# Kernel tuning notes

Measured on AMD Instinct MI355X. Metric: run time of the kernel, lower is better.

The kernel has to match this reference:

```python
import jax, jax.numpy as jnp
import numpy as np
from functools import partial

DN = ('NCHW', 'OIHW', 'NCHW')

def _conv(x, w, b, stride, pad):
    y = jax.lax.conv_general_dilated(x, w, (stride, stride), [(pad, pad), (pad, pad)], dimension_numbers=DN)
    return y + b[None, :, None, None]

def _leaky(x, s):
    return jnp.where(x >= 0, x, s * x)

def _lstm_gates(pre, c):
    # PyTorch gate order: i, f, g, o
    i, f, g, o = jnp.split(pre, 4, axis=-1)
    c_new = jax.nn.sigmoid(f) * c + jax.nn.sigmoid(i) * jnp.tanh(g)
    h_new = jax.nn.sigmoid(o) * jnp.tanh(c_new)
    return h_new, c_new

def setup_inputs() -> dict:
    key = jax.random.key(0)
    ks = iter(jax.random.split(key, 32))
    s = 0.05
    d = {}
    d['x'] = jax.random.normal(next(ks), (128, 3, 64, 64), jnp.float32)
    # conv stack params
    d['w1'] = jax.random.normal(next(ks), (64, 3, 7, 7)) * s;   d['b1'] = jnp.zeros((64,))
    d['w2'] = jax.random.normal(next(ks), (128, 64, 7, 7)) * s; d['b2'] = jnp.zeros((128,))
    d['w3'] = jax.random.normal(next(ks), (256, 128, 5, 5)) * s; d['b3'] = jnp.zeros((256,))
    d['w4'] = jax.random.normal(next(ks), (512, 256, 5, 5)) * s; d['b4'] = jnp.zeros((512,))
    d['w5'] = jax.random.normal(next(ks), (512, 512, 5, 5)) * s; d['b5'] = jnp.zeros((512,))
    # 2-layer LSTM (hidden=512), PyTorch layout: W_ih [4H, In], W_hh [4H, H]
    H = 512
    for l in range(2):
        d[f'wih{l}'] = jax.random.normal(next(ks), (4 * H, H)) * s
        d[f'whh{l}'] = jax.random.normal(next(ks), (4 * H, H)) * s
        d[f'bih{l}'] = jnp.zeros((4 * H,))
        d[f'bhh{l}'] = jnp.zeros((4 * H,))
    # FC head
    d['fw1'] = jax.random.normal(next(ks), (512, 512)) * s; d['fb1'] = jnp.zeros((512,))
    d['fw2'] = jax.random.normal(next(ks), (13, 512)) * s;  d['fb2'] = jnp.zeros((13,))
    return d

TIMESTEPS = 20

def reference(x, w1, b1, w2, b2, w3, b3, w4, b4, w5, b5,
              wih0, whh0, bih0, bhh0, wih1, whh1, bih1, bhh1,
              fw1, fb1, fw2, fb2):
    B = x.shape[0]
    h = _conv(x, w1, b1, 2, 3); h = _leaky(h, 0.2)
    h = _conv(h, w2, b2, 2, 0); h = _leaky(h, 0.2)
    h = _conv(h, w3, b3, 1, 0); h = _leaky(h, 0.2)
    h = _conv(h, w4, b4, 1, 0); h = _leaky(h, 0.2)
    h = _conv(h, w5, b5, 1, 0); h = _leaky(h, 0.2)
    feat = h.reshape(B, -1)  # [B, 512]
    H = 512
    # input to layer-0 is constant across timesteps: precompute Wx once
    xW0 = feat @ wih0.T + bih0 + bhh0  # [B, 4H]
    zeros = jnp.zeros((B, H), feat.dtype)

    def step(carry, _):
        h0, c0, h1, c1 = carry
        h0n, c0n = _lstm_gates(xW0 + h0 @ whh0.T, c0)
        pre1 = h0n @ wih1.T + bih1 + bhh1 + h1 @ whh1.T
        h1n, c1n = _lstm_gates(pre1, c1)
        return (h0n, c0n, h1n, c1n), h1n

    _, ys = jax.lax.scan(step, (zeros, zeros, zeros, zeros), None, length=TIMESTEPS)
    y = ys.reshape(TIMESTEPS * B, H)
    y = _leaky(y @ fw1.T + fb1, 0.01)
    y = jax.nn.sigmoid(y @ fw2.T + fb2)
    return y
```

## Files before the change

### kernel.cpp

```cpp
#include <hip/hip_runtime.h>
#include <math.h>

typedef _Float16 half_t;
typedef __attribute__((ext_vector_type(8))) _Float16 f16x8;
typedef __attribute__((ext_vector_type(4))) _Float16 f16x4;
typedef __attribute__((ext_vector_type(4))) float f32x4;

#define LEAKY(v, s) ((v) >= 0.f ? (v) : (s) * (v))

__device__ __forceinline__ float sig_(float x) { return 1.f / (1.f + expf(-x)); }
__device__ __forceinline__ half_t f2h(float f) { return (half_t)f; }

#define GLD(gp, lp)                                              \
  __builtin_amdgcn_global_load_lds(                              \
      (const __attribute__((address_space(1))) void*)(gp),       \
      (__attribute__((address_space(3))) void*)(lp), 16, 0, 0)

#define PHASE_WAIT(N)                                            \
  asm volatile("s_waitcnt vmcnt(" #N ")" ::: "memory");          \
  __builtin_amdgcn_s_barrier();                                  \
  __builtin_amdgcn_sched_barrier(0)

#define QOFF0 2048LL
#define QOFF1 4096LL
#define QOFF2 135168LL
#define QOFF3 266240LL
#define QOFF4 5283840LL
#define QOFF5 5310464LL
#define QOFF6 6359040LL
#define QOFF7 6621184LL
#define QOFF8 7669760LL
#define QOFF9 9766912LL

__global__ void prep_all(
    const float* __restrict__ x, const float* __restrict__ w1,
    const float* __restrict__ wih0, const float* __restrict__ whh0,
    const float* __restrict__ bih0, const float* __restrict__ bhh0,
    const float* __restrict__ wih1, const float* __restrict__ whh1,
    const float* __restrict__ bih1, const float* __restrict__ bhh1,
    const float* __restrict__ fw1,
    float* __restrict__ bg0, float* __restrict__ bg1,
    float* __restrict__ czero, unsigned* __restrict__ hzero,
    half_t* __restrict__ xpad, half_t* __restrict__ w1r,
    half_t* __restrict__ wih0h, half_t* __restrict__ fw1h,
    half_t* __restrict__ wcat0h, half_t* __restrict__ wcat1h) {
  long long i = (long long)blockIdx.x * blockDim.x + threadIdx.x;
  if (i < QOFF0) {
    bg0[i] = bih0[i] + bhh0[i];
  } else if (i < QOFF1) {
    long long j = i - QOFF0;
    bg1[j] = bih1[j] + bhh1[j];
  } else if (i < QOFF2) {
    czero[i - QOFF1] = 0.f;
  } else if (i < QOFF3) {
    hzero[i - QOFF2] = 0u;
  } else if (i < QOFF4) {
    long long j = i - QOFF3;
    int c = j & 7;
    long long t = j >> 3;
    int iw = t % 70; t /= 70;
    int ih = t % 70;
    int n = t / 70;
    float v = 0.f;
    if (c < 3 && ih >= 3 && ih < 67 && iw >= 3 && iw < 67)
      v = x[((n * 3 + c) * 64 + (ih - 3)) * 64 + (iw - 3)];
    xpad[j] = f2h(v);
  } else if (i < QOFF5) {
    int j = (int)(i - QOFF4);
    int kg = j % 416, co = j / 416;
    int ci = kg & 7, tap = kg >> 3;
    float v = 0.f;
    if (tap < 49 && ci < 3) {
      int kh = tap / 7, kw = tap % 7;
      v = w1[((co * 3 + ci) * 7 + kh) * 7 + kw];
    }
    w1r[j] = f2h(v);
  } else if (i < QOFF6) {
    int j = (int)(i - QOFF5);
    wih0h[j] = f2h(wih0[j]);
  } else if (i < QOFF7) {
    int j = (int)(i - QOFF6);
    fw1h[j] = f2h(fw1[j]);
  } else if (i < QOFF8) {
    int j = (int)(i - QOFF7);
    int r = j >> 9, k = j & 511;
    int u = r >> 2, g = r & 3;
    wcat0h[j] = f2h(whh0[(g * 512 + u) * 512 + k]);
  } else if (i < QOFF9) {
    int j = (int)(i - QOFF8);
    int r = j >> 10, k = j & 1023;
    int u = r >> 2, g = r & 3;
    int row = g * 512 + u;
    wcat1h[j] = f2h(k < 512 ? wih1[row * 512 + k] : whh1[row * 512 + (k - 512)]);
  }
}

__global__ __launch_bounds__(256) void prep_wT(
    const float* __restrict__ w2, const float* __restrict__ w3,
    const float* __restrict__ w4, const float* __restrict__ w5,
    half_t* __restrict__ w2r, half_t* __restrict__ w3r,
    half_t* __restrict__ w4r, half_t* __restrict__ w5r) {
  __shared__ float T[12800];
  int bid = blockIdx.x, tid = threadIdx.x;
  const float* W;
  half_t* D;
  int co, Cin, TAP, lg2;
  if (bid < 128) {
    W = w2; D = w2r; co = bid; Cin = 64; TAP = 49; lg2 = 6;
  } else if (bid < 384) {
    W = w3; D = w3r; co = bid - 128; Cin = 128; TAP = 25; lg2 = 7;
  } else if (bid < 896) {
    W = w4; D = w4r; co = bid - 384; Cin = 256; TAP = 25; lg2 = 8;
  } else {
    W = w5; D = w5r; co = bid - 896; Cin = 512; TAP = 25; lg2 = 9;
  }
  int n = Cin * TAP;
  const float* src = W + (size_t)co * n;
  for (int i = tid; i < n; i += 256) T[i] = src[i];
  __syncthreads();
  half_t* dst = D + (size_t)co * n;
  for (int j = tid; j < n; j += 256) {
    int ci = j & (Cin - 1);
    int tap = j >> lg2;
    dst[j] = f2h(T[ci * TAP + tap]);
  }
}

template <int KW, int S, int LOG2CIN, int OUTMODE>
__global__ __launch_bounds__(256) void conv_mfma(
    const half_t* __restrict__ xin, const half_t* __restrict__ wr,
    const float* __restrict__ bias, void* __restrict__ outp,
    int Hin, int Win, int Hout, int Wout, int Cout, int K, int ktiles, float slope,
    long long zstride) {
  constexpr int CIN = 1 << LOG2CIN;
  __shared__ half_t lds[4][4096];
  const int tid = threadIdx.x;
  const int lane = tid & 63, wid = tid >> 6;
  const int sRow = tid >> 2, sCh = tid & 3;
  const int sSwz = sCh ^ ((sRow ^ (sRow >> 2)) & 3);
  const int kt0 = blockIdx.z * ktiles;
  const half_t* gArow = wr + (size_t)(blockIdx.y * 64 + sRow) * K + sSwz * 8;
  int p = blockIdx.x * 64 + sRow;
  int hw = Hout * Wout;
  int n = p / hw;
  int rem = p - n * hw;
  int oh = rem / Wout;
  int ow = rem - oh * Wout;
  const half_t* xb = xin + ((size_t)(n * Hin + oh * S) * Win + ow * S) * CIN;
  const int fr = lane & 15, fc = lane >> 4;
  const int r0 = (wid & 1) * 32, c0 = (wid >> 1) * 32;
  const int sw = (fc ^ ((fr ^ (fr >> 2)) & 3)) * 8;
  const int ia0 = (r0 + fr) * 32 + sw;
  const int ia1 = (r0 + 16 + fr) * 32 + sw;
  const int ib0 = 2048 + (c0 + fr) * 32 + sw;
  const int ib1 = 2048 + (c0 + 16 + fr) * 32 + sw;

  auto stage = [&](int t, int buf) {
    GLD(gArow + (size_t)(kt0 + t) * 32, &lds[buf][wid * 512]);
    int kg = (kt0 + t) * 32 + sSwz * 8;
    int ci = kg & (CIN - 1);
    int tap = kg >> LOG2CIN;
    int kh = tap / KW, kw = tap - kh * KW;
    GLD(xb + (kh * Win + kw) * CIN + ci, &lds[buf][2048 + wid * 512]);
  };

  f32x4 acc00 = {0.f, 0.f, 0.f, 0.f};
  f32x4 acc01 = acc00, acc10 = acc00, acc11 = acc00;

// ... 5 lines not shown
    f16x8 b1 = *(const f16x8*)&L[ib1];
    acc00 = __builtin_amdgcn_mfma_f32_16x16x32_f16(a0, b0, acc00, 0, 0, 0);
    acc01 = __builtin_amdgcn_mfma_f32_16x16x32_f16(a0, b1, acc01, 0, 0, 0);
    acc10 = __builtin_amdgcn_mfma_f32_16x16x32_f16(a1, b0, acc10, 0, 0, 0);
    acc11 = __builtin_amdgcn_mfma_f32_16x16x32_f16(a1, b1, acc11, 0, 0, 0);
  };

  stage(0, 0);
  stage(1, 1);
  stage(2, 2);
  int t = 0;
  for (; t < ktiles - 3; ++t) {
    PHASE_WAIT(4);
    stage(t + 3, (t + 3) & 3);
    compute(t & 3);
  }
  PHASE_WAIT(4);
  compute(t & 3);
  ++t;
  PHASE_WAIT(2);
  compute(t & 3);
  ++t;
  PHASE_WAIT(0);
  compute(t & 3);

#pragma unroll
  for (int am = 0; am < 2; ++am) {
#pragma unroll
    for (int bn = 0; bn < 2; ++bn) {
      f32x4 a = am == 0 ? (bn == 0 ? acc00 : acc01) : (bn == 0 ? acc10 : acc11);
      int co = blockIdx.y * 64 + r0 + am * 16 + fc * 4;
      int px = blockIdx.x * 64 + c0 + bn * 16 + fr;
      size_t o = (size_t)px * Cout + co;
      if (OUTMODE == 2) {
        float* pb = (float*)outp + (size_t)blockIdx.z * zstride;
        *(f32x4*)&pb[o] = a;
      } else {
        f32x4 bb = *(const f32x4*)&bias[co];
        f32x4 v;
#pragma unroll
        for (int j = 0; j < 4; ++j) {
          float tt = a[j] + bb[j];
          v[j] = LEAKY(tt, slope);
        }
        if (OUTMODE == 1) {
          *(f32x4*)&((float*)outp)[o] = v;
        } else {
          f16x4 hv;
#pragma unroll
          for (int j = 0; j < 4; ++j) hv[j] = f2h(v[j]);
          *(f16x4*)&((half_t*)outp)[o] = hv;
        }
      }
    }
  }
}

template <int KW, int S, int LOG2CIN, int OUTMODE>
__global__ __launch_bounds__(256) void conv_mfma128(
    const half_t* __restrict__ xin, const half_t* __restrict__ wr,
    const float* __restrict__ bias, void* __restrict__ outp,
    int Hin, int Win, int Hout, int Wout, int Cout, int K, int ktiles, float slope,
    long long zstride, int Y, int G) {
  constexpr int CIN = 1 << LOG2CIN;
  __shared__ half_t lds[4][8192];
  const int L = blockIdx.x;
  const int bx = L / G;
  const int g = L % G;
  const int by = g % Y;
  const int bz = g / Y;
  const int tid = threadIdx.x;
  const int lane = tid & 63, wid = tid >> 6;
  const int sRow = tid >> 2, sCh = tid & 3;
  const int sSwz = sCh ^ ((sRow ^ (sRow >> 2)) & 3);
  const int kt0 = bz * ktiles;
  const half_t* gA0 = wr + (size_t)(by * 128 + sRow) * K + sSwz * 8;
  const half_t* gA1 = wr + (size_t)(by * 128 + 64 + sRow) * K + sSwz * 8;
  int hw = Hout * Wout;
  int p0 = bx * 128 + sRow;
  int n0 = p0 / hw, r0p = p0 - n0 * hw, oh0 = r0p / Wout, ow0 = r0p - oh0 * Wout;
  const half_t* xb0 = xin + ((size_t)(n0 * Hin + oh0 * S) * Win + ow0 * S) * CIN;
  int p1 = p0 + 64;
  int n1 = p1 / hw, r1p = p1 - n1 * hw, oh1 = r1p / Wout, ow1 = r1p - oh1 * Wout;
  const half_t* xb1 = xin + ((size_t)(n1 * Hin + oh1 * S) * Win + ow1 * S) * CIN;

  const int fr = lane & 15, fc = lane >> 4;
  const int wr_ = wid & 1, wc_ = wid >> 1;
  const int sw = (fc ^ ((fr ^ (fr >> 2)) & 3)) * 8;
  const int iaB = (wr_ * 64 + fr) * 32 + sw;
  const int ibB = 4096 + (wc_ * 64 + fr) * 32 + sw;

  auto stage = [&](int t, int buf) {
    half_t* LB = &lds[buf][0];
    GLD(gA0 + (size_t)(kt0 + t) * 32, LB + wid * 512);
    GLD(gA1 + (size_t)(kt0 + t) * 32, LB + 2048 + wid * 512);
    int kg = (kt0 + t) * 32 + sSwz * 8;
    int ci = kg & (CIN - 1);
    int tap = kg >> LOG2CIN;
// ... 18 lines not shown
    for (int fj = 0; fj < 4; ++fj) b[fj] = *(const f16x8*)&L2[ibB + fj * 512];
#pragma unroll
    for (int fi = 0; fi < 4; ++fi)
#pragma unroll
      for (int fj = 0; fj < 4; ++fj)
        acc[fi][fj] = __builtin_amdgcn_mfma_f32_16x16x32_f16(a[fi], b[fj], acc[fi][fj], 0, 0, 0);
  };

  stage(0, 0);
  stage(1, 1);
  stage(2, 2);
  int t = 0;
  for (; t < ktiles - 3; ++t) {
    PHASE_WAIT(8);
    stage(t + 3, (t + 3) & 3);
    compute(t & 3);
  }
  PHASE_WAIT(8);
  compute(t & 3);
  ++t;
  PHASE_WAIT(4);
  compute(t & 3);
  ++t;
  PHASE_WAIT(0);
  compute(t & 3);

#pragma unroll
  for (int fi = 0; fi < 4; ++fi) {
#pragma unroll
    for (int fj = 0; fj < 4; ++fj) {
      int co = by * 128 + wr_ * 64 + fi * 16 + fc * 4;
      int px = bx * 128 + wc_ * 64 + fj * 16 + fr;
      size_t o = (size_t)px * Cout + co;
      if (OUTMODE == 3) {
        half_t* pb = (half_t*)outp + (size_t)bz * zstride;
        f16x4 hv;
#pragma unroll
        for (int j = 0; j < 4; ++j) hv[j] = f2h(acc[fi][fj][j]);
        *(f16x4*)&pb[o] = hv;
      } else {
        f32x4 bb = *(const f32x4*)&bias[co];
        f16x4 hv;
#pragma unroll
        for (int j = 0; j < 4; ++j) {
          float tt = acc[fi][fj][j] + bb[j];
          hv[j] = f2h(LEAKY(tt, slope));
        }
        *(f16x4*)&((half_t*)outp)[o] = hv;
      }
    }
  }
}

__global__ void finalize_part(const float* __restrict__ pb, const float* __restrict__ bias,
                              half_t* __restrict__ out, int size, int nz) {
  int i = blockIdx.x * blockDim.x + threadIdx.x;
  if (i >= size) return;
  float s = bias[i & 511];
  for (int z = 0; z < nz; ++z) s += pb[(size_t)z * size + i];
  out[i] = f2h(LEAKY(s, 0.2f));
}

__global__ void finalize_h(const half_t* __restrict__ pb, const float* __restrict__ bias,
                           half_t* __restrict__ out, int size8, int nz, int cmask,
                           long long zstride) {
  int idx = blockIdx.x * blockDim.x + threadIdx.x;
  if (idx >= size8) return;
  long long i = (long long)idx * 8;
  float s[8];
#pragma unroll
  for (int q = 0; q < 8; ++q) s[q] = bias[(int)((i + q) & cmask)];
  for (int z = 0; z < nz; ++z) {
    f16x8 v = *(const f16x8*)&pb[(size_t)z * zstride + i];
#pragma unroll
    for (int q = 0; q < 8; ++q) s[q] += (float)v[q];
  }
  f16x8 o;
#pragma unroll
  for (int q = 0; q < 8; ++q) o[q] = f2h(LEAKY(s[q], 0.2f));
  *(f16x8*)&out[i] = o;
}

__global__ __launch_bounds__(256) void lstm_fused(
    const half_t* __restrict__ h0in, half_t* __restrict__ h0out,
    const half_t* __restrict__ h1in, half_t* __restrict__ h1out,
    const half_t* __restrict__ wcat0, const half_t* __restrict__ wcat1,
    const float* __restrict__ xw0, const float* __restrict__ bg1,
    float* __restrict__ c0, float* __restrict__ c1,
    half_t* __restrict__ ysout, int zl1, int zfc,
    const half_t* __restrict__ fcw, const float* __restrict__ fcb,
    const half_t* __restrict__ fcin, half_t* __restrict__ fcout) {
  const int bzp = blockIdx.z;
  const bool isFC = (bzp == zfc);
  const bool isL1 = (bzp == zl1);
  if (isFC && blockIdx.y >= 8) return;
  const int NT = isL1 ? 16 : 8;
  const half_t* Asrc = isFC ? fcw : (isL1 ? wcat1 : wcat0);
  const int K = NT * 64;

  __shared__ half_t lds[4][8192];
  const int tid = threadIdx.x;
  const int lane = tid & 63, wid = tid >> 6;
  const int ybase = blockIdx.y * 64, bbase = blockIdx.x * 64;
  const int rA0 = wid * 16 + (lane >> 3);
  const int rA1 = rA0 + 8;
  const int chS = ((lane & 7) ^ ((lane >> 3) & 7)) * 8;
  const half_t* gA0 = Asrc + (size_t)(ybase + rA0) * K + chS;
  const half_t* gA1 = Asrc + (size_t)(ybase + rA1) * K + chS;
  const size_t hb0 = (size_t)(bbase + rA0) * 512 + chS;
  const size_t hb1 = (size_t)(bbase + rA1) * 512 + chS;
  const half_t* bsrc0 = isFC ? fcin : h0in;

  auto stage = [&](int t, int buf) {
    GLD(gA0 + t * 64, &lds[buf][wid * 1024]);
    GLD(gA1 + t * 64, &lds[buf][wid * 1024 + 512]);
    const half_t* hs = (isL1 && t >= 8) ? h1in : bsrc0;
    int koff = (isL1 && t >= 8) ? (t - 8) * 64 : t * 64;
    GLD(hs + hb0 + koff, &lds[buf][4096 + wid * 1024]);
    GLD(hs + hb1 + koff, &lds[buf][4096 + wid * 1024 + 512]);
  };
// ... 47 lines not shown
  ++t;
  PHASE_WAIT(0);
  compute(t & 3);

  if (isFC) {
#pragma unroll
    for (int fi = 0; fi < 2; ++fi) {
#pragma unroll
      for (int fj = 0; fj < 2; ++fj) {
        int Rb = ybase + wr_ * 32 + fi * 16 + fc * 4;
        int b = bbase + wc_ * 32 + fj * 16 + fr;
        f32x4 bb = *(const f32x4*)&fcb[Rb];
        f16x4 hv;
#pragma unroll
        for (int j = 0; j < 4; ++j) {
          float tt = acc[fi][fj][j] + bb[j];
          hv[j] = f2h(LEAKY(tt, 0.01f));
        }
        *(f16x4*)&fcout[(size_t)b * 512 + Rb] = hv;
      }
    }
    return;
  }

  float* c = isL1 ? c1 : c0;
  half_t* hout = isL1 ? h1out : h0out;
#pragma unroll
  for (int fi = 0; fi < 2; ++fi) {
#pragma unroll
    for (int fj = 0; fj < 2; ++fj) {
      int Rb = ybase + wr_ * 32 + fi * 16 + fc * 4;
      int u = Rb >> 2;
      int b = bbase + wc_ * 32 + fj * 16 + fr;
      float p[4];
#pragma unroll
      for (int j = 0; j < 4; ++j) {
        float s = acc[fi][fj][j];
        s += isL1 ? bg1[j * 512 + u] : xw0[b * 2048 + j * 512 + u];
        p[j] = s;
      }
      int ci = b * 512 + u;
      float cprev = c[ci];
      float ig = sig_(p[0]);
      float fg = sig_(p[1]);
      float gg = tanhf(p[2]);
      float og = sig_(p[3]);
      float cn = fg * cprev + ig * gg;
      float hn = og * tanhf(cn);
      c[ci] = cn;
      hout[ci] = f2h(hn);
      if (isL1) ysout[ci] = f2h(hn);
    }
  }
}

__global__ void fc2_sigmoid(const half_t* __restrict__ in, const float* __restrict__ w,
                            const float* __restrict__ b, float* __restrict__ out) {
  int idx = blockIdx.x * blockDim.x + threadIdx.x;
  if (idx >= 2560 * 13) return;
  int j = idx % 13, r = idx / 13;
  const half_t* ip = in + (size_t)r * 512;
  const float* wp = w + j * 512;
  float s = b[j];
  for (int k = 0; k < 512; k += 8) {
    f16x8 hv = *(const f16x8*)&ip[k];
#pragma unroll
    for (int q = 0; q < 8; ++q) s = fmaf((float)hv[q], wp[k + q], s);
  }
  out[idx] = sig_(s);
}

extern "C" void kernel_launch(void* const* d_in, const int* in_sizes, int n_in,
                              void* d_out, int out_size, void* d_ws, size_t ws_size,
                              hipStream_t stream) {
  const float* x   = (const float*)d_in[0];
  const float* w1  = (const float*)d_in[1];  const float* b1 = (const float*)d_in[2];
  const float* w2  = (const float*)d_in[3];  const float* b2 = (const float*)d_in[4];
  const float* w3  = (const float*)d_in[5];  const float* b3 = (const float*)d_in[6];
  const float* w4  = (const float*)d_in[7];  const float* b4 = (const float*)d_in[8];
  const float* w5  = (const float*)d_in[9];  const float* b5 = (const float*)d_in[10];
  const float* wih0 = (const float*)d_in[11]; const float* whh0 = (const float*)d_in[12];
  const float* bih0 = (const float*)d_in[13]; const float* bhh0 = (const float*)d_in[14];
  const float* wih1 = (const float*)d_in[15]; const float* whh1 = (const float*)d_in[16];
  const float* bih1 = (const float*)d_in[17]; const float* bhh1 = (const float*)d_in[18];
  const float* fw1 = (const float*)d_in[19]; const float* fb1 = (const float*)d_in[20];
  const float* fw2 = (const float*)d_in[21]; const float* fb2 = (const float*)d_in[22];
  float* out = (float*)d_out;

  float* bg0 = (float*)d_ws;
  float* bg1 = bg0 + 2048;
  float* xw0 = bg1 + 2048;
  float* c0  = xw0 + 262144;
  float* c1  = c0 + 65536;
  half_t* h0a = (half_t*)(c1 + 65536);
  half_t* h0b = h0a + 65536;
  half_t* h1a = h0b + 65536;
  half_t* h1b = h1a + 65536;
  half_t* BUF1 = h1b + 65536;
  half_t* BUF2 = BUF1 + 8388608;
  half_t* w1r  = BUF2 + 2768896;
  half_t* w2r  = w1r + 26624;
  half_t* w3r  = w2r + 401408;
  half_t* w4r  = w3r + 819200;
  half_t* w5r  = w4r + 3276800;
  half_t* wih0h  = w5r + 6553600;
  half_t* wcat0h = wih0h + 1048576;
  half_t* wcat1h = wcat0h + 1048576;
  half_t* fw1h   = wcat1h + 2097152;
  half_t* xpad   = fw1h + 262144;
  half_t* pbH = xpad;
  float* pbC = (float*)xpad;

  half_t* A1 = BUF1;
  half_t* A2 = BUF2;
  half_t* A3 = BUF1;
  half_t* A4 = BUF2;
  half_t* feat = BUF1;
  half_t* ys   = BUF2;
  half_t* fc1o = BUF2 + 1310720;

  dim3 blk(256);

  prep_all<<<38152, blk, 0, stream>>>(
      x, w1, wih0, whh0, bih0, bhh0, wih1, whh1, bih1, bhh1, fw1,
      bg0, bg1, c0, (unsigned*)h0a, xpad, w1r, wih0h, fw1h, wcat0h, wcat1h);
  prep_wT<<<1408, blk, 0, stream>>>(w2, w3, w4, w5, w2r, w3r, w4r, w5r);

  conv_mfma<7, 2, 3, 0><<<dim3(2048, 1, 1), blk, 0, stream>>>(
      xpad, w1r, b1, A1, 70, 70, 32, 32, 64, 416, 13, 0.2f, 0);
  conv_mfma128<7, 2, 6, 3><<<338, blk, 0, stream>>>(
      A1, w2r, b2, pbH, 32, 32, 13, 13, 128, 3136, 49, 0.2f, 2768896LL, 1, 2);
  finalize_h<<<1352, blk, 0, stream>>>(pbH, b2, A2, 346112, 2, 127, 2768896LL);
  conv_mfma128<5, 1, 7, 3><<<324, blk, 0, stream>>>(
      A2, w3r, b3, pbH, 13, 13, 9, 9, 256, 3200, 50, 0.2f, 2654208LL, 2, 4);
  finalize_h<<<1296, blk, 0, stream>>>(pbH, b3, A3, 331776, 2, 255, 2654208LL);
  conv_mfma128<5, 1, 8, 3><<<400, blk, 0, stream>>>(
      A3, w4r, b4, pbH, 9, 9, 5, 5, 512, 6400, 50, 0.2f, 1638400LL, 4, 16);
  finalize_h<<<800, blk, 0, stream>>>(pbH, b4, A4, 204800, 4, 511, 1638400LL);
  conv_mfma<5, 1, 9, 2><<<dim3(2, 8, 25), blk, 0, stream>>>(
      A4, w5r, b5, pbC, 5, 5, 1, 1, 512, 12800, 16, 0.2f, (long long)65536);
  finalize_part<<<256, blk, 0, stream>>>(pbC, b5, feat, 65536, 25);

  conv_mfma<1, 1, 9, 1><<<dim3(2, 32, 1), blk, 0, stream>>>(
      feat, wih0h, bg0, xw0, 1, 1, 1, 1, 2048, 512, 16, 1.0f, 0);

  half_t* h0buf[2] = {h0a, h0b};
  half_t* h1buf[2] = {h1a, h1b};
  lstm_fused<<<dim3(2, 32, 1), blk, 0, stream>>>(
      h0a, h0b, h1a, h1a, wcat0h, wcat1h, xw0, bg1, c0, c1, ys,
      -1, -1, fw1h, fb1, nullptr, nullptr);
  lstm_fused<<<dim3(2, 32, 2), blk, 0, stream>>>(
      h0buf[1], h0buf[0], h1buf[0], h1buf[1], wcat0h, wcat1h, xw0, bg1, c0, c1,
      ys, 1, -1, fw1h, fb1, nullptr, nullptr);
  for (int t = 3; t <= 20; ++t) {
    lstm_fused<<<dim3(2, 32, 3), blk, 0, stream>>>(
        h0buf[(t - 1) & 1], h0buf[t & 1], h1buf[t & 1], h1buf[(t - 1) & 1],
        wcat0h, wcat1h, xw0, bg1, c0, c1, ys + (size_t)(t - 2) * 65536,
        1, 2, fw1h, fb1, ys + (size_t)(t - 3) * 65536, fc1o + (size_t)(t - 3) * 65536);
  }
  lstm_fused<<<dim3(2, 32, 2), blk, 0, stream>>>(
      h0buf[0], h0buf[1], h1buf[1], h1buf[0],
      wcat0h, wcat1h, xw0, bg1, c0, c1, ys + (size_t)19 * 65536,
      0, 1, fw1h, fb1, ys + (size_t)18 * 65536, fc1o + (size_t)18 * 65536);

  conv_mfma<1, 1, 9, 0><<<dim3(2, 8, 1), blk, 0, stream>>>(
      ys + (size_t)19 * 65536, fw1h, fb1, fc1o + (size_t)19 * 65536,
      1, 1, 1, 1, 512, 512, 16, 0.01f, 0);
  fc2_sigmoid<<<130, blk, 0, stream>>>(fc1o, fw2, fb2, out);
}
```

Baseline: 403.1 us.

## Fuse split-K reduction into conv kernels via atomic last-block finalize

Removes the separate finalize kernels after each split-K conv. Each block writes its partial, then bumps a per-tile atomic counter, and the last block to arrive sums all partials, adds bias and applies leaky ReLU. Also merges the two prep kernels into one launch, which zeroes the counters. This saves several kernel launches and the gaps between them. In exchange it adds fences, atomics and a serialized reduction tail in the last-arriving block of each tile.

Result: slower. 699.5 us (+73.5%).

```diff
diff --git a/kernel.cpp b/kernel.cpp
--- a/kernel.cpp
+++ b/kernel.cpp
@@ -21,19 +21,23 @@
   __builtin_amdgcn_s_barrier();                                  \
   __builtin_amdgcn_sched_barrier(0)
 
-#define QOFF0 2048LL
-#define QOFF1 4096LL
-#define QOFF2 135168LL
-#define QOFF3 266240LL
-#define QOFF4 5283840LL
-#define QOFF5 5310464LL
-#define QOFF6 6359040LL
-#define QOFF7 6621184LL
-#define QOFF8 7669760LL
-#define QOFF9 9766912LL
-
-__global__ void prep_all(
+#define R0 2048LL
+#define R1 4096LL
+#define R2 135168LL
+#define R3 266240LL
+#define R4 266688LL
+#define R5 5284288LL
+#define R6 5310912LL
+#define R7 6359488LL
+#define R8 6621632LL
+#define R9 7670208LL
+#define R10 9767360LL
+#define ELEM_BLOCKS 38154
+
+__global__ __launch_bounds__(256) void prep_main(
     const float* __restrict__ x, const float* __restrict__ w1,
+    const float* __restrict__ w2, const float* __restrict__ w3,
+    const float* __restrict__ w4, const float* __restrict__ w5,
     const float* __restrict__ wih0, const float* __restrict__ whh0,
     const float* __restrict__ bih0, const float* __restrict__ bhh0,
     const float* __restrict__ wih1, const float* __restrict__ whh1,
@@ -41,21 +45,54 @@
     const float* __restrict__ fw1,
     float* __restrict__ bg0, float* __restrict__ bg1,
     float* __restrict__ czero, unsigned* __restrict__ hzero,
+    unsigned* __restrict__ cntz,
     half_t* __restrict__ xpad, half_t* __restrict__ w1r,
+    half_t* __restrict__ w2r, half_t* __restrict__ w3r,
+    half_t* __restrict__ w4r, half_t* __restrict__ w5r,
     half_t* __restrict__ wih0h, half_t* __restrict__ fw1h,
     half_t* __restrict__ wcat0h, half_t* __restrict__ wcat1h) {
-  long long i = (long long)blockIdx.x * blockDim.x + threadIdx.x;
-  if (i < QOFF0) {
+  __shared__ float T[12800];
+  const int tid = threadIdx.x;
+  if (blockIdx.x >= ELEM_BLOCKS) {
+    int bid = blockIdx.x - ELEM_BLOCKS;
+    const float* W;
+    half_t* D;
+    int co, Cin, TAP, lg2;
+    if (bid < 128) {
+      W = w2; D = w2r; co = bid; Cin = 64; TAP = 49; lg2 = 6;
+    } else if (bid < 384) {
+      W = w3; D = w3r; co = bid - 128; Cin = 128; TAP = 25; lg2 = 7;
+    } else if (bid < 896) {
+      W = w4; D = w4r; co = bid - 384; Cin = 256; TAP = 25; lg2 = 8;
+    } else {
+      W = w5; D = w5r; co = bid - 896; Cin = 512; TAP = 25; lg2 = 9;
+    }
+    int n = Cin * TAP;
+    const float* src = W + (size_t)co * n;
+    for (int i = tid; i < n; i += 256) T[i] = src[i];
+    __syncthreads();
+    half_t* dst = D + (size_t)co * n;
+    for (int j = tid; j < n; j += 256) {
+      int ci = j & (Cin - 1);
+      int tap = j >> lg2;
+      dst[j] = f2h(T[ci * TAP + tap]);
+    }
+    return;
+  }
+  long long i = (long long)blockIdx.x * 256 + tid;
+  if (i < R0) {
     bg0[i] = bih0[i] + bhh0[i];
-  } else if (i < QOFF1) {
-    long long j = i - QOFF0;
+  } else if (i < R1) {
+    long long j = i - R0;
     bg1[j] = bih1[j] + bhh1[j];
-  } else if (i < QOFF2) {
-    czero[i - QOFF1] = 0.f;
-  } else if (i < QOFF3) {
-    hzero[i - QOFF2] = 0u;
-  } else if (i < QOFF4) {
-    long long j = i - QOFF3;
+  } else if (i < R2) {
+    czero[i - R1] = 0.f;
+  } else if (i < R3) {
+    hzero[i - R2] = 0u;
+  } else if (i < R4) {
+    cntz[i - R3] = 0u;
+  } else if (i < R5) {
+    long long j = i - R4;
     int c = j & 7;
     long long t = j >> 3;
     int iw = t % 70; t /= 70;
@@ -65,8 +102,8 @@
     if (c < 3 && ih >= 3 && ih < 67 && iw >= 3 && iw < 67)
       v = x[((n * 3 + c) * 64 + (ih - 3)) * 64 + (iw - 3)];
     xpad[j] = f2h(v);
-  } else if (i < QOFF5) {
-    int j = (int)(i - QOFF4);
+  } else if (i < R6) {
+    int j = (int)(i - R5);
     int kg = j % 416, co = j / 416;
     int ci = kg & 7, tap = kg >> 3;
     float v = 0.f;
@@ -75,54 +112,23 @@
       v = w1[((co * 3 + ci) * 7 + kh) * 7 + kw];
     }
     w1r[j] = f2h(v);
-  } else if (i < QOFF6) {
-    int j = (int)(i - QOFF5);
+  } else if (i < R7) {
+    int j = (int)(i - R6);
     wih0h[j] = f2h(wih0[j]);
-  } else if (i < QOFF7) {
-    int j = (int)(i - QOFF6);
+  } else if (i < R8) {
+    int j = (int)(i - R7);
     fw1h[j] = f2h(fw1[j]);
-  } else if (i < QOFF8) {
-    int j = (int)(i - QOFF7);
+  } else if (i < R9) {
+    int j = (int)(i - R8);
     int r = j >> 9, k = j & 511;
     int u = r >> 2, g = r & 3;
     wcat0h[j] = f2h(whh0[(g * 512 + u) * 512 + k]);
-  } else if (i < QOFF9) {
-    int j = (int)(i - QOFF8);
+  } else if (i < R10) {
+    int j = (int)(i - R9);
     int r = j >> 10, k = j & 1023;
     int u = r >> 2, g = r & 3;
     int row = g * 512 + u;
     wcat1h[j] = f2h(k < 512 ? wih1[row * 512 + k] : whh1[row * 512 + (k - 512)]);
-  }
-}
-
-__global__ __launch_bounds__(256) void prep_wT(
-    const float* __restrict__ w2, const float* __restrict__ w3,
-    const float* __restrict__ w4, const float* __restrict__ w5,
-    half_t* __restrict__ w2r, half_t* __restrict__ w3r,
-    half_t* __restrict__ w4r, half_t* __restrict__ w5r) {
-  __shared__ float T[12800];
-  int bid = blockIdx.x, tid = threadIdx.x;
-  const float* W;
-  half_t* D;
-  int co, Cin, TAP, lg2;
-  if (bid < 128) {
-    W = w2; D = w2r; co = bid; Cin = 64; TAP = 49; lg2 = 6;
-  } else if (bid < 384) {
-    W = w3; D = w3r; co = bid - 128; Cin = 128; TAP = 25; lg2 = 7;
-  } else if (bid < 896) {
-    W = w4; D = w4r; co = bid - 384; Cin = 256; TAP = 25; lg2 = 8;
-  } else {
-    W = w5; D = w5r; co = bid - 896; Cin = 512; TAP = 25; lg2 = 9;
-  }
-  int n = Cin * TAP;
-  const float* src = W + (size_t)co * n;
-  for (int i = tid; i < n; i += 256) T[i] = src[i];
-  __syncthreads();
-  half_t* dst = D + (size_t)co * n;
-  for (int j = tid; j < n; j += 256) {
-    int ci = j & (Cin - 1);
-    int tap = j >> lg2;
-    dst[j] = f2h(T[ci * TAP + tap]);
   }
 }
 
@@ -131,9 +137,10 @@
     const half_t* __restrict__ xin, const half_t* __restrict__ wr,
     const float* __restrict__ bias, void* __restrict__ outp,
     int Hin, int Win, int Hout, int Wout, int Cout, int K, int ktiles, float slope,
-    long long zstride) {
+    long long zstride, void* pbuf, unsigned* cnt, int Z) {
   constexpr int CIN = 1 << LOG2CIN;
   __shared__ half_t lds[4][4096];
+  __shared__ unsigned lastf;
   const int tid = threadIdx.x;
   const int lane = tid & 63, wid = tid >> 6;
   const int sRow = tid >> 2, sCh = tid & 3;
@@ -205,9 +212,9 @@
       int co = blockIdx.y * 64 + r0 + am * 16 + fc * 4;
       int px = blockIdx.x * 64 + c0 + bn * 16 + fr;
       size_t o = (size_t)px * Cout + co;
-      if (OUTMODE == 2) {
-        float* pb = (float*)outp + (size_t)blockIdx.z * zstride;
-        *(f32x4*)&pb[o] = a;
+      if (OUTMODE == 4) {
+        float* myp = (float*)pbuf + (size_t)blockIdx.z * zstride;
+        *(f32x4*)&myp[o] = a;
       } else {
         f32x4 bb = *(const f32x4*)&bias[co];
         f32x4 v;
@@ -227,6 +234,37 @@
       }
     }
   }
+
+  if (OUTMODE == 4) {
+    __threadfence();
+    if (tid == 0) {
+      unsigned c = __hip_atomic_fetch_add(cnt + (blockIdx.x * gridDim.y + blockIdx.y),
+                                          1u, __ATOMIC_ACQ_REL, __HIP_MEMORY_SCOPE_AGENT);
+      lastf = (c == (unsigned)(Z - 1)) ? 1u : 0u;
+    }
+    __syncthreads();
+    if (!lastf) return;
+    half_t* outh = (half_t*)outp;
+#pragma unroll
+    for (int am = 0; am < 2; ++am) {
+#pragma unroll
+      for (int bn = 0; bn < 2; ++bn) {
+        int co = blockIdx.y * 64 + r0 + am * 16 + fc * 4;
+        int px = blockIdx.x * 64 + c0 + bn * 16 + fr;
+        size_t o = (size_t)px * Cout + co;
+        f32x4 s = *(const f32x4*)&bias[co];
+        for (int z = 0; z < Z; ++z) {
+          f32x4 pv = *(const f32x4*)&((float*)pbuf)[(size_t)z * zstride + o];
+#pragma unroll
+          for (int j = 0; j < 4; ++j) s[j] += pv[j];
+        }
+        f16x4 hv;
+#pragma unroll
+        for (int j = 0; j < 4; ++j) hv[j] = f2h(LEAKY(s[j], slope));
+        *(f16x4*)&outh[o] = hv;
+      }
+    }
+  }
 }
 
 template <int KW, int S, int LOG2CIN, int OUTMODE>
@@ -234,9 +272,10 @@
     const half_t* __restrict__ xin, const half_t* __restrict__ wr,
     const float* __restrict__ bias, void* __restrict__ outp,
     int Hin, int Win, int Hout, int Wout, int Cout, int K, int ktiles, float slope,
-    long long zstride, int Y, int G) {
+    long long zstride, int Y, int G, void* pbuf, unsigned* cnt, int Z) {
   constexpr int CIN = 1 << LOG2CIN;
   __shared__ half_t lds[4][8192];
+  __shared__ unsigned lastf;
   const int L = blockIdx.x;
   const int bx = L / G;
   const int g = L % G;
@@ -321,12 +360,12 @@
       int co = by * 128 + wr_ * 64 + fi * 16 + fc * 4;
       int px = bx * 128 + wc_ * 64 + fj * 16 + fr;
       size_t o = (size_t)px * Cout + co;
-      if (OUTMODE == 3) {
-        half_t* pb = (half_t*)outp + (size_t)bz * zstride;
+      if (OUTMODE == 4) {
+        half_t* myp = (half_t*)pbuf + (size_t)bz * zstride;
         f16x4 hv;
 #pragma unroll
         for (int j = 0; j < 4; ++j) hv[j] = f2h(acc[fi][fj][j]);
-        *(f16x4*)&pb[o] = hv;
+        *(f16x4*)&myp[o] = hv;
       } else {
         f32x4 bb = *(const f32x4*)&bias[co];
         f16x4 hv;
@@ -339,35 +378,37 @@
       }
     }
   }
-}
-
-__global__ void finalize_part(const float* __restrict__ pb, const float* __restrict__ bias,
-                              half_t* __restrict__ out, int size, int nz) {
-  int i = blockIdx.x * blockDim.x + threadIdx.x;
-  if (i >= size) return;
-  float s = bias[i & 511];
-  for (int z = 0; z < nz; ++z) s += pb[(size_t)z * size + i];
-  out[i] = f2h(LEAKY(s, 0.2f));
-}
-
-__global__ void finalize_h(const half_t* __restrict__ pb, const float* __restrict__ bias,
-                           half_t* __restrict__ out, int size8, int nz, int cmask,
-                           long long zstride) {
-  int idx = blockIdx.x * blockDim.x + threadIdx.x;
-  if (idx >= size8) return;
-  long long i = (long long)idx * 8;
-  float s[8];
-#pragma unroll
-  for (int q = 0; q < 8; ++q) s[q] = bias[(int)((i + q) & cmask)];
-  for (int z = 0; z < nz; ++z) {
-    f16x8 v = *(const f16x8*)&pb[(size_t)z * zstride + i];
-#pragma unroll
-    for (int q = 0; q < 8; ++q) s[q] += (float)v[q];
-  }
-  f16x8 o;
-#pragma unroll
-  for (int q = 0; q < 8; ++q) o[q] = f2h(LEAKY(s[q], 0.2f));
-  *(f16x8*)&out[i] = o;
+
+  if (OUTMODE == 4) {
+    __threadfence();
+    if (tid == 0) {
+      unsigned c = __hip_atomic_fetch_add(cnt + (bx * Y + by), 1u,
+                                          __ATOMIC_ACQ_REL, __HIP_MEMORY_SCOPE_AGENT);
+      lastf = (c == (unsigned)(Z - 1)) ? 1u : 0u;
+    }
+    __syncthreads();
+    if (!lastf) return;
+    half_t* outh = (half_t*)outp;
+#pragma unroll
+    for (int fi = 0; fi < 4; ++fi) {
+#pragma unroll
+      for (int fj = 0; fj < 4; ++fj) {
+        int co = by * 128 + wr_ * 64 + fi * 16 + fc * 4;
+        int px = bx * 128 + wc_ * 64 + fj * 16 + fr;
+        size_t o = (size_t)px * Cout + co;
+        f32x4 s = *(const f32x4*)&bias[co];
+        for (int z = 0; z < Z; ++z) {
+          f16x4 pv = *(const f16x4*)&((half_t*)pbuf)[(size_t)z * zstride + o];
+#pragma unroll
+          for (int j = 0; j < 4; ++j) s[j] += (float)pv[j];
+        }
+        f16x4 hv;
+#pragma unroll
+        for (int j = 0; j < 4; ++j) hv[j] = f2h(LEAKY(s[j], slope));
+        *(f16x4*)&outh[o] = hv;
+      }
+    }
+  }
 }
 
 __global__ __launch_bounds__(256) void lstm_fused(
@@ -563,9 +604,14 @@
   half_t* wcat0h = wih0h + 1048576;
   half_t* wcat1h = wcat0h + 1048576;
   half_t* fw1h   = wcat1h + 2097152;
-  half_t* xpad   = fw1h + 262144;
+  unsigned* cntU = (unsigned*)(fw1h + 262144);
+  half_t* xpad   = (half_t*)(cntU + 448);
   half_t* pbH = xpad;
   float* pbC = (float*)xpad;
+  unsigned* cntA = cntU;
+  unsigned* cntB = cntU + 169;
+  unsigned* cntC = cntU + 331;
+  unsigned* cntD = cntU + 431;
 
   half_t* A1 = BUF1;
   half_t* A2 = BUF2;
@@ -577,28 +623,28 @@
 
   dim3 blk(256);
 
-  prep_all<<<38152, blk, 0, stream>>>(
-      x, w1, wih0, whh0, bih0, bhh0, wih1, whh1, bih1, bhh1, fw1,
-      bg0, bg1, c0, (unsigned*)h0a, xpad, w1r, wih0h, fw1h, wcat0h, wcat1h);
-  prep_wT<<<1408, blk, 0, stream>>>(w2, w3, w4, w5, w2r, w3r, w4r, w5r);
+  prep_main<<<ELEM_BLOCKS + 1408, blk, 0, stream>>>(
+      x, w1, w2, w3, w4, w5, wih0, whh0, bih0, bhh0, wih1, whh1, bih1, bhh1, fw1,
+      bg0, bg1, c0, (unsigned*)h0a, cntU, xpad, w1r, w2r, w3r, w4r, w5r,
+      wih0h, fw1h, wcat0h, wcat1h);
 
   conv_mfma<7, 2, 3, 0><<<dim3(2048, 1, 1), blk, 0, stream>>>(
-      xpad, w1r, b1, A1, 70, 70, 32, 32, 64, 416, 13, 0.2f, 0);
-  conv_mfma128<7, 2, 6, 3><<<338, blk, 0, stream>>>(
-      A1, w2r, b2, pbH, 32, 32, 13, 13, 128, 3136, 49, 0.2f, 2768896LL, 1, 2);
-  finalize_h<<<1352, blk, 0, stream>>>(pbH, b2, A2, 346112, 2, 127, 2768896LL);
-  conv_mfma128<5, 1, 7, 3><<<324, blk, 0, stream>>>(
-      A2, w3r, b3, pbH, 13, 13, 9, 9, 256, 3200, 50, 0.2f, 2654208LL, 2, 4);
-  finalize_h<<<1296, blk, 0, stream>>>(pbH, b3, A3, 331776, 2, 255, 2654208LL);
-  conv_mfma128<5, 1, 8, 3><<<400, blk, 0, stream>>>(
-      A3, w4r, b4, pbH, 9, 9, 5, 5, 512, 6400, 50, 0.2f, 1638400LL, 4, 16);
-  finalize_h<<<800, blk, 0, stream>>>(pbH, b4, A4, 204800, 4, 511, 1638400LL);
-  conv_mfma<5, 1, 9, 2><<<dim3(2, 8, 25), blk, 0, stream>>>(
-      A4, w5r, b5, pbC, 5, 5, 1, 1, 512, 12800, 16, 0.2f, (long long)65536);
-  finalize_part<<<256, blk, 0, stream>>>(pbC, b5, feat, 65536, 25);
+      xpad, w1r, b1, A1, 70, 70, 32, 32, 64, 416, 13, 0.2f, 0, nullptr, nullptr, 0);
+  conv_mfma128<7, 2, 6, 4><<<338, blk, 0, stream>>>(
+      A1, w2r, b2, A2, 32, 32, 13, 13, 128, 3136, 49, 0.2f, 2768896LL, 1, 2,
+      pbH, cntA, 2);
+  conv_mfma128<5, 1, 7, 4><<<324, blk, 0, stream>>>(
+      A2, w3r, b3, A3, 13, 13, 9, 9, 256, 3200, 50, 0.2f, 2654208LL, 2, 4,
+      pbH, cntB, 2);
+  conv_mfma128<5, 1, 8, 4><<<400, blk, 0, stream>>>(
+      A3, w4r, b4, A4, 9, 9, 5, 5, 512, 6400, 50, 0.2f, 1638400LL, 4, 16,
+      pbH, cntC, 4);
+  conv_mfma<5, 1, 9, 4><<<dim3(2, 8, 25), blk, 0, stream>>>(
+      A4, w5r, b5, feat, 5, 5, 1, 1, 512, 12800, 16, 0.2f, 65536LL,
+      pbC, cntD, 25);
 
   conv_mfma<1, 1, 9, 1><<<dim3(2, 32, 1), blk, 0, stream>>>(
-      feat, wih0h, bg0, xw0, 1, 1, 1, 1, 2048, 512, 16, 1.0f, 0);
+      feat, wih0h, bg0, xw0, 1, 1, 1, 1, 2048, 512, 16, 1.0f, 0, nullptr, nullptr, 0);
 
   half_t* h0buf[2] = {h0a, h0b};
   half_t* h1buf[2] = {h1a, h1b};
@@ -621,6 +667,6 @@
 
   conv_mfma<1, 1, 9, 0><<<dim3(2, 8, 1), blk, 0, stream>>>(
       ys + (size_t)19 * 65536, fw1h, fb1, fc1o + (size_t)19 * 65536,
-      1, 1, 1, 1, 512, 512, 16, 0.01f, 0);
+      1, 1, 1, 1, 512, 512, 16, 0.01f, 0, nullptr, nullptr, 0);
   fc2_sigmoid<<<130, blk, 0, stream>>>(fc1o, fw2, fb2, out);
 }
```

## Merge prep kernels and fuse input projection with first LSTM step

Applied to the files above, without the earlier changes.

Folds the weight-transpose prep kernel into the elementwise prep kernel so one launch does both. Replaces the separate xW0 GEMM plus first lstm_fused launch with a dedicated lstm0_step kernel. That kernel computes the input projection, stores it in gate-interleaved layout, and applies the t=0 gate math directly, using c_prev=0 and h_prev=0. Bias and xw0 are reordered into gate-interleaved layout so the LSTM epilogue can load four gates with one vector load instead of four strided scalar loads. This removes two launches and one pass over the hidden state, at the cost of a larger, heavier prep kernel.

New measurement: 401.6 us. No clear change (-0.4%).

```diff
diff --git a/kernel.cpp b/kernel.cpp
--- a/kernel.cpp
+++ b/kernel.cpp
@@ -21,41 +21,77 @@
   __builtin_amdgcn_s_barrier();                                  \
   __builtin_amdgcn_sched_barrier(0)
 
-#define QOFF0 2048LL
-#define QOFF1 4096LL
-#define QOFF2 135168LL
-#define QOFF3 266240LL
-#define QOFF4 5283840LL
-#define QOFF5 5310464LL
-#define QOFF6 6359040LL
-#define QOFF7 6621184LL
-#define QOFF8 7669760LL
-#define QOFF9 9766912LL
-
-__global__ void prep_all(
+#define R0 2048LL
+#define R1 4096LL
+#define R2 135168LL
+#define R3 266240LL
+#define R4 5283840LL
+#define R5 5310464LL
+#define R6 6359040LL
+#define R7 6621184LL
+#define R8 7669760LL
+#define R9 9766912LL
+#define ELEM_BLOCKS 38152
+
+__global__ __launch_bounds__(256) void prep_main(
     const float* __restrict__ x, const float* __restrict__ w1,
+    const float* __restrict__ w2, const float* __restrict__ w3,
+    const float* __restrict__ w4, const float* __restrict__ w5,
     const float* __restrict__ wih0, const float* __restrict__ whh0,
     const float* __restrict__ bih0, const float* __restrict__ bhh0,
     const float* __restrict__ wih1, const float* __restrict__ whh1,
     const float* __restrict__ bih1, const float* __restrict__ bhh1,
     const float* __restrict__ fw1,
-    float* __restrict__ bg0, float* __restrict__ bg1,
+    float* __restrict__ bg0c, float* __restrict__ bg1c,
     float* __restrict__ czero, unsigned* __restrict__ hzero,
     half_t* __restrict__ xpad, half_t* __restrict__ w1r,
-    half_t* __restrict__ wih0h, half_t* __restrict__ fw1h,
+    half_t* __restrict__ w2r, half_t* __restrict__ w3r,
+    half_t* __restrict__ w4r, half_t* __restrict__ w5r,
+    half_t* __restrict__ wih0c, half_t* __restrict__ fw1h,
     half_t* __restrict__ wcat0h, half_t* __restrict__ wcat1h) {
-  long long i = (long long)blockIdx.x * blockDim.x + threadIdx.x;
-  if (i < QOFF0) {
-    bg0[i] = bih0[i] + bhh0[i];
-  } else if (i < QOFF1) {
-    long long j = i - QOFF0;
-    bg1[j] = bih1[j] + bhh1[j];
-  } else if (i < QOFF2) {
-    czero[i - QOFF1] = 0.f;
-  } else if (i < QOFF3) {
-    hzero[i - QOFF2] = 0u;
-  } else if (i < QOFF4) {
-    long long j = i - QOFF3;
+  __shared__ float T[12800];
+  const int tid = threadIdx.x;
+  if (blockIdx.x >= ELEM_BLOCKS) {
+    int bid = blockIdx.x - ELEM_BLOCKS;
+    const float* W;
+    half_t* D;
+    int co, Cin, TAP, lg2;
+    if (bid < 128) {
+      W = w2; D = w2r; co = bid; Cin = 64; TAP = 49; lg2 = 6;
+    } else if (bid < 384) {
+      W = w3; D = w3r; co = bid - 128; Cin = 128; TAP = 25; lg2 = 7;
+    } else if (bid < 896) {
+      W = w4; D = w4r; co = bid - 384; Cin = 256; TAP = 25; lg2 = 8;
+    } else {
+      W = w5; D = w5r; co = bid - 896; Cin = 512; TAP = 25; lg2 = 9;
+    }
+    int n = Cin * TAP;
+    const float* src = W + (size_t)co * n;
+    for (int i = tid; i < n; i += 256) T[i] = src[i];
+    __syncthreads();
+    half_t* dst = D + (size_t)co * n;
+    for (int j = tid; j < n; j += 256) {
+      int ci = j & (Cin - 1);
+      int tap = j >> lg2;
+      dst[j] = f2h(T[ci * TAP + tap]);
+    }
+    return;
+  }
+  long long i = (long long)blockIdx.x * 256 + tid;
+  if (i < R0) {
+    int j = (int)i;
+    int u = j >> 2, g = j & 3;
+    bg0c[j] = bih0[g * 512 + u] + bhh0[g * 512 + u];
+  } else if (i < R1) {
+    int j = (int)(i - R0);
+    int u = j >> 2, g = j & 3;
+    bg1c[j] = bih1[g * 512 + u] + bhh1[g * 512 + u];
+  } else if (i < R2) {
+    czero[i - R1] = 0.f;
+  } else if (i < R3) {
+    hzero[i - R2] = 0u;
+  } else if (i < R4) {
+    long long j = i - R3;
     int c = j & 7;
     long long t = j >> 3;
     int iw = t % 70; t /= 70;
@@ -65,8 +101,8 @@
     if (c < 3 && ih >= 3 && ih < 67 && iw >= 3 && iw < 67)
       v = x[((n * 3 + c) * 64 + (ih - 3)) * 64 + (iw - 3)];
     xpad[j] = f2h(v);
-  } else if (i < QOFF5) {
-    int j = (int)(i - QOFF4);
+  } else if (i < R5) {
+    int j = (int)(i - R4);
     int kg = j % 416, co = j / 416;
     int ci = kg & 7, tap = kg >> 3;
     float v = 0.f;
@@ -75,54 +111,25 @@
       v = w1[((co * 3 + ci) * 7 + kh) * 7 + kw];
     }
     w1r[j] = f2h(v);
-  } else if (i < QOFF6) {
-    int j = (int)(i - QOFF5);
-    wih0h[j] = f2h(wih0[j]);
-  } else if (i < QOFF7) {
-    int j = (int)(i - QOFF6);
+  } else if (i < R6) {
+    int j = (int)(i - R5);
+    int r = j >> 9, k = j & 511;
+    int u = r >> 2, g = r & 3;
+    wih0c[j] = f2h(wih0[(g * 512 + u) * 512 + k]);
+  } else if (i < R7) {
+    int j = (int)(i - R6);
     fw1h[j] = f2h(fw1[j]);
-  } else if (i < QOFF8) {
-    int j = (int)(i - QOFF7);
+  } else if (i < R8) {
+    int j = (int)(i - R7);
     int r = j >> 9, k = j & 511;
     int u = r >> 2, g = r & 3;
     wcat0h[j] = f2h(whh0[(g * 512 + u) * 512 + k]);
-  } else if (i < QOFF9) {
-    int j = (int)(i - QOFF8);
+  } else if (i < R9) {
+    int j = (int)(i - R8);
     int r = j >> 10, k = j & 1023;
     int u = r >> 2, g = r & 3;
     int row = g * 512 + u;
     wcat1h[j] = f2h(k < 512 ? wih1[row * 512 + k] : whh1[row * 512 + (k - 512)]);
-  }
-}
-
-__global__ __launch_bounds__(256) void prep_wT(
-    const float* __restrict__ w2, const float* __restrict__ w3,
-    const float* __restrict__ w4, const float* __restrict__ w5,
-    half_t* __restrict__ w2r, half_t* __restrict__ w3r,
-    half_t* __restrict__ w4r, half_t* __restrict__ w5r) {
-  __shared__ float T[12800];
-  int bid = blockIdx.x, tid = threadIdx.x;
-  const float* W;
-  half_t* D;
-  int co, Cin, TAP, lg2;
-  if (bid < 128) {
-    W = w2; D = w2r; co = bid; Cin = 64; TAP = 49; lg2 = 6;
-  } else if (bid < 384) {
-    W = w3; D = w3r; co = bid - 128; Cin = 128; TAP = 25; lg2 = 7;
-  } else if (bid < 896) {
-    W = w4; D = w4r; co = bid - 384; Cin = 256; TAP = 25; lg2 = 8;
-  } else {
-    W = w5; D = w5r; co = bid - 896; Cin = 512; TAP = 25; lg2 = 9;
-  }
-  int n = Cin * TAP;
-  const float* src = W + (size_t)co * n;
-  for (int i = tid; i < n; i += 256) T[i] = src[i];
-  __syncthreads();
-  half_t* dst = D + (size_t)co * n;
-  for (int j = tid; j < n; j += 256) {
-    int ci = j & (Cin - 1);
-    int tap = j >> lg2;
-    dst[j] = f2h(T[ci * TAP + tap]);
   }
 }
 
@@ -210,20 +217,13 @@
         *(f32x4*)&pb[o] = a;
       } else {
         f32x4 bb = *(const f32x4*)&bias[co];
-        f32x4 v;
+        f16x4 hv;
 #pragma unroll
         for (int j = 0; j < 4; ++j) {
           float tt = a[j] + bb[j];
-          v[j] = LEAKY(tt, slope);
+          hv[j] = f2h(LEAKY(tt, slope));
         }
-        if (OUTMODE == 1) {
-          *(f32x4*)&((float*)outp)[o] = v;
-        } else {
-          f16x4 hv;
-#pragma unroll
-          for (int j = 0; j < 4; ++j) hv[j] = f2h(v[j]);
-          *(f16x4*)&((half_t*)outp)[o] = hv;
-        }
+        *(f16x4*)&((half_t*)outp)[o] = hv;
       }
     }
   }
@@ -370,11 +370,106 @@
   *(f16x8*)&out[i] = o;
 }
 
+__global__ __launch_bounds__(256) void lstm0_step(
+    const half_t* __restrict__ feat, const half_t* __restrict__ wih0c,
+    const float* __restrict__ bg0c, float* __restrict__ xw0c,
+    float* __restrict__ c0, half_t* __restrict__ h0out) {
+  __shared__ half_t lds[4][8192];
+  const int tid = threadIdx.x;
+  const int lane = tid & 63, wid = tid >> 6;
+  const int ybase = blockIdx.y * 64, bbase = blockIdx.x * 64;
+  const int rA0 = wid * 16 + (lane >> 3);
+  const int rA1 = rA0 + 8;
+  const int chS = ((lane & 7) ^ ((lane >> 3) & 7)) * 8;
+  const half_t* gA0 = wih0c + (size_t)(ybase + rA0) * 512 + chS;
+  const half_t* gA1 = wih0c + (size_t)(ybase + rA1) * 512 + chS;
+  const size_t hb0 = (size_t)(bbase + rA0) * 512 + chS;
+  const size_t hb1 = (size_t)(bbase + rA1) * 512 + chS;
+
+  auto stage = [&](int t, int buf) {
+    GLD(gA0 + t * 64, &lds[buf][wid * 1024]);
+    GLD(gA1 + t * 64, &lds[buf][wid * 1024 + 512]);
+    GLD(feat + hb0 + t * 64, &lds[buf][4096 + wid * 1024]);
+    GLD(feat + hb1 + t * 64, &lds[buf][4096 + wid * 1024 + 512]);
+  };
+
+  const int fr = lane & 15, fc = lane >> 4;
+  const int wr_ = wid & 1, wc_ = wid >> 1;
+
+  f32x4 acc[2][2];
+#pragma unroll
+  for (int fi = 0; fi < 2; ++fi)
+#pragma unroll
+    for (int fj = 0; fj < 2; ++fj) acc[fi][fj] = (f32x4){0.f, 0.f, 0.f, 0.f};
+
+  auto compute = [&](int buf) {
+    const half_t* L = &lds[buf][0];
+#pragma unroll
+    for (int s = 0; s < 2; ++s) {
+      f16x8 a[2], b[2];
+#pragma unroll
+      for (int fi = 0; fi < 2; ++fi) {
+        int row = wr_ * 32 + fi * 16 + fr;
+        a[fi] = *(const f16x8*)&L[row * 64 + (((s * 4 + fc) ^ (fr & 7)) * 8)];
+      }
+#pragma unroll
+      for (int fj = 0; fj < 2; ++fj) {
+        int brow = wc_ * 32 + fj * 16 + fr;
+        b[fj] = *(const f16x8*)&L[4096 + brow * 64 + (((s * 4 + fc) ^ (fr & 7)) * 8)];
+      }
+#pragma unroll
+      for (int fi = 0; fi < 2; ++fi)
+#pragma unroll
+        for (int fj = 0; fj < 2; ++fj)
+          acc[fi][fj] = __builtin_amdgcn_mfma_f32_16x16x32_f16(a[fi], b[fj], acc[fi][fj], 0, 0, 0);
+    }
+  };
+
+  stage(0, 0);
+  stage(1, 1);
+  stage(2, 2);
+  int t = 0;
+  for (; t < 5; ++t) {
+    PHASE_WAIT(8);
+    stage(t + 3, (t + 3) & 3);
+    compute(t & 3);
+  }
+  PHASE_WAIT(8);
+  compute(5 & 3);
+  PHASE_WAIT(4);
+  compute(6 & 3);
+  PHASE_WAIT(0);
+  compute(7 & 3);
+
+#pragma unroll
+  for (int fi = 0; fi < 2; ++fi) {
+#pragma unroll
+    for (int fj = 0; fj < 2; ++fj) {
+      int Rb = ybase + wr_ * 32 + fi * 16 + fc * 4;
+      int u = Rb >> 2;
+      int b = bbase + wc_ * 32 + fj * 16 + fr;
+      f32x4 bb = *(const f32x4*)&bg0c[Rb];
+      f32x4 pre;
+#pragma unroll
+      for (int j = 0; j < 4; ++j) pre[j] = acc[fi][fj][j] + bb[j];
+      *(f32x4*)&xw0c[(size_t)b * 2048 + Rb] = pre;
+      float ig = sig_(pre[0]);
+      float gg = tanhf(pre[2]);
+      float og = sig_(pre[3]);
+      float cn = ig * gg;
+      float hn = og * tanhf(cn);
+      int ci = b * 512 + u;
+      c0[ci] = cn;
+      h0out[ci] = f2h(hn);
+    }
+  }
+}
+
 __global__ __launch_bounds__(256) void lstm_fused(
     const half_t* __restrict__ h0in, half_t* __restrict__ h0out,
     const half_t* __restrict__ h1in, half_t* __restrict__ h1out,
     const half_t* __restrict__ wcat0, const half_t* __restrict__ wcat1,
-    const float* __restrict__ xw0, const float* __restrict__ bg1,
+    const float* __restrict__ xw0c, const float* __restrict__ bg1c,
     float* __restrict__ c0, float* __restrict__ c1,
     half_t* __restrict__ ysout, int zl1, int zfc,
     const half_t* __restrict__ fcw, const float* __restrict__ fcb,
@@ -488,13 +583,11 @@
       int Rb = ybase + wr_ * 32 + fi * 16 + fc * 4;
       int u = Rb >> 2;
       int b = bbase + wc_ * 32 + fj * 16 + fr;
+      f32x4 bb = isL1 ? *(const f32x4*)&bg1c[Rb]
+                      : *(const f32x4*)&xw0c[(size_t)b * 2048 + Rb];
       float p[4];
 #pragma unroll
-      for (int j = 0; j < 4; ++j) {
-        float s = acc[fi][fj][j];
-        s += isL1 ? bg1[j * 512 + u] : xw0[b * 2048 + j * 512 + u];
-        p[j] = s;
-      }
+      for (int j = 0; j < 4; ++j) p[j] = acc[fi][fj][j] + bb[j];
       int ci = b * 512 + u;
       float cprev = c[ci];
       float ig = sig_(p[0]);
@@ -543,10 +636,10 @@
   const float* fw2 = (const float*)d_in[21]; const float* fb2 = (const float*)d_in[22];
   float* out = (float*)d_out;
 
-  float* bg0 = (float*)d_ws;
-  float* bg1 = bg0 + 2048;
-  float* xw0 = bg1 + 2048;
-  float* c0  = xw0 + 262144;
+  float* bg0c = (float*)d_ws;
+  float* bg1c = bg0c + 2048;
+  float* xw0c = bg1c + 2048;
+  float* c0  = xw0c + 262144;
   float* c1  = c0 + 65536;
   half_t* h0a = (half_t*)(c1 + 65536);
   half_t* h0b = h0a + 65536;
@@ -559,8 +652,8 @@
   half_t* w3r  = w2r + 401408;
   half_t* w4r  = w3r + 819200;
   half_t* w5r  = w4r + 3276800;
-  half_t* wih0h  = w5r + 6553600;
-  half_t* wcat0h = wih0h + 1048576;
+  half_t* wih0ch = w5r + 6553600;
+  half_t* wcat0h = wih0ch + 1048576;
   half_t* wcat1h = wcat0h + 1048576;
   half_t* fw1h   = wcat1h + 2097152;
   half_t* xpad   = fw1h + 262144;
@@ -577,10 +670,10 @@
 
   dim3 blk(256);
 
-  prep_all<<<38152, blk, 0, stream>>>(
-      x, w1, wih0, whh0, bih0, bhh0, wih1, whh1, bih1, bhh1, fw1,
-      bg0, bg1, c0, (unsigned*)h0a, xpad, w1r, wih0h, fw1h, wcat0h, wcat1h);
-  prep_wT<<<1408, blk, 0, stream>>>(w2, w3, w4, w5, w2r, w3r, w4r, w5r);
+  prep_main<<<ELEM_BLOCKS + 1408, blk, 0, stream>>>(
+      x, w1, w2, w3, w4, w5, wih0, whh0, bih0, bhh0, wih1, whh1, bih1, bhh1, fw1,
+      bg0c, bg1c, c0, (unsigned*)h0a, xpad, w1r, w2r, w3r, w4r, w5r,
+      wih0ch, fw1h, wcat0h, wcat1h);
 
   conv_mfma<7, 2, 3, 0><<<dim3(2048, 1, 1), blk, 0, stream>>>(
       xpad, w1r, b1, A1, 70, 70, 32, 32, 64, 416, 13, 0.2f, 0);
@@ -594,29 +687,25 @@
       A3, w4r, b4, pbH, 9, 9, 5, 5, 512, 6400, 50, 0.2f, 1638400LL, 4, 16);
   finalize_h<<<800, blk, 0, stream>>>(pbH, b4, A4, 204800, 4, 511, 1638400LL);
   conv_mfma<5, 1, 9, 2><<<dim3(2, 8, 25), blk, 0, stream>>>(
-      A4, w5r, b5, pbC, 5, 5, 1, 1, 512, 12800, 16, 0.2f, (long long)65536);
+      A4, w5r, b5, pbC, 5, 5, 1, 1, 512, 12800, 16, 0.2f, 65536LL);
   finalize_part<<<256, blk, 0, stream>>>(pbC, b5, feat, 65536, 25);
-
-  conv_mfma<1, 1, 9, 1><<<dim3(2, 32, 1), blk, 0, stream>>>(
-      feat, wih0h, bg0, xw0, 1, 1, 1, 1, 2048, 512, 16, 1.0f, 0);
 
   half_t* h0buf[2] = {h0a, h0b};
   half_t* h1buf[2] = {h1a, h1b};
-  lstm_fused<<<dim3(2, 32, 1), blk, 0, stream>>>(
-      h0a, h0b, h1a, h1a, wcat0h, wcat1h, xw0, bg1, c0, c1, ys,
-      -1, -1, fw1h, fb1, nullptr, nullptr);
+  lstm0_step<<<dim3(2, 32), blk, 0, stream>>>(feat, wih0ch, bg0c, xw0c, c0, h0b);
+
   lstm_fused<<<dim3(2, 32, 2), blk, 0, stream>>>(
-      h0buf[1], h0buf[0], h1buf[0], h1buf[1], wcat0h, wcat1h, xw0, bg1, c0, c1,
+      h0buf[1], h0buf[0], h1buf[0], h1buf[1], wcat0h, wcat1h, xw0c, bg1c, c0, c1,
       ys, 1, -1, fw1h, fb1, nullptr, nullptr);
   for (int t = 3; t <= 20; ++t) {
     lstm_fused<<<dim3(2, 32, 3), blk, 0, stream>>>(
         h0buf[(t - 1) & 1], h0buf[t & 1], h1buf[t & 1], h1buf[(t - 1) & 1],
-        wcat0h, wcat1h, xw0, bg1, c0, c1, ys + (size_t)(t - 2) * 65536,
+        wcat0h, wcat1h, xw0c, bg1c, c0, c1, ys + (size_t)(t - 2) * 65536,
         1, 2, fw1h, fb1, ys + (size_t)(t - 3) * 65536, fc1o + (size_t)(t - 3) * 65536);
   }
   lstm_fused<<<dim3(2, 32, 2), blk, 0, stream>>>(
       h0buf[0], h0buf[1], h1buf[1], h1buf[0],
-      wcat0h, wcat1h, xw0, bg1, c0, c1, ys + (size_t)19 * 65536,
+      wcat0h, wcat1h, xw0c, bg1c, c0, c1, ys + (size_t)19 * 65536,
       0, 1, fw1h, fb1, ys + (size_t)18 * 65536, fc1o + (size_t)18 * 65536);
 
   conv_mfma<1, 1, 9, 0><<<dim3(2, 8, 1), blk, 0, stream>>>(
```
